# Performance work log

Hardware: AMD Instinct MI355X
Metric: run time of the kernel (lower is better)

## Reference

```python
import jax, jax.numpy as jnp
import numpy as np

B, L, D = 2, 2048, 1024
H, DH = 16, 64
SCALE = 1.0 / np.sqrt(DH).astype(np.float32)
NEG = -1e9


def setup_inputs() -> dict:
    key = jax.random.key(0)
    ks = jax.random.split(key, 12)
    s = 0.02
    x = jax.random.normal(ks[0], (B, L, D), jnp.float32)
    lattice = jax.random.normal(ks[1], (B, 6), jnp.float32)
    B_graph = jax.random.normal(ks[2], (B, L, L), jnp.float32) * 0.05
    # causal additive mask [L, L]
    attn_mask = jnp.where(jnp.tril(jnp.ones((L, L), bool)), 0.0, NEG).astype(jnp.float32)
    Wq = jax.random.normal(ks[3], (D, H * DH), jnp.float32) * s
    bq = jnp.zeros((H * DH,), jnp.float32)
    Wk = jax.random.normal(ks[4], (D, H * DH), jnp.float32) * s
    bk = jnp.zeros((H * DH,), jnp.float32)
    Wv = jax.random.normal(ks[5], (D, H * DH), jnp.float32) * s
    bv = jnp.zeros((H * DH,), jnp.float32)
    Wo = jax.random.normal(ks[6], (H * DH, D), jnp.float32) * s
    bo = jnp.zeros((D,), jnp.float32)
    Wl = jax.random.normal(ks[7], (6, H), jnp.float32) * s
    bl = jnp.zeros((H,), jnp.float32)
    return {"x": x, "lattice": lattice, "B_graph": B_graph, "attn_mask": attn_mask,
            "Wq": Wq, "bq": bq, "Wk": Wk, "bk": bk, "Wv": Wv, "bv": bv,
            "Wo": Wo, "bo": bo, "Wl": Wl, "bl": bl}


def reference(x, lattice, B_graph, attn_mask, Wq, bq, Wk, bk, Wv, bv, Wo, bo, Wl, bl):
    b, l, d = x.shape
    # projections -> [b, h, l, dh]
    q = (x @ Wq + bq).reshape(b, l, H, DH).transpose(0, 2, 1, 3)
    k = (x @ Wk + bk).reshape(b, l, H, DH).transpose(0, 2, 1, 3)
    v = (x @ Wv + bv).reshape(b, l, H, DH).transpose(0, 2, 1, 3)
    scores = jnp.einsum('bhid,bhjd->bhij', q, k) * SCALE
    lattice_bias = lattice @ Wl + bl          # [b, h]
    scores = scores + lattice_bias[:, :, None, None]
    scores = scores + B_graph[:, None, :, :]   # [b,1,l,l]
    scores = scores + attn_mask[None, None, :, :]
    attn = jax.nn.softmax(scores.astype(jnp.float32), axis=-1).astype(scores.dtype)
    out = jnp.einsum('bhij,bhjd->bhid', attn, v)
    out = out.transpose(0, 2, 1, 3).reshape(b, l, H * DH)
    out = out @ Wo + bo
    return (out, attn)
```

## Files before the change

kernel.cpp:

```cpp
#include <hip/hip_runtime.h>
#include <stdint.h>
#include <stddef.h>

#define BB 2
#define LL 2048
#define DD 1024
#define HH 16
#define DHH 64
#define NH 1024

typedef __attribute__((ext_vector_type(8))) __bf16 bf16x8;
typedef __attribute__((ext_vector_type(4))) float f32x4;

__device__ __forceinline__ f32x4 mfma_bf16(bf16x8 a, bf16x8 b, f32x4 c) {
    return __builtin_amdgcn_mfma_f32_16x16x32_bf16(a, b, c, 0, 0, 0);
}

__device__ __forceinline__ unsigned short f2bf(float f) {
    union { float f; unsigned u; } v; v.f = f;
    unsigned r = v.u + 0x7FFFu + ((v.u >> 16) & 1u);
    return (unsigned short)(r >> 16);
}

__device__ __forceinline__ float bf2f(unsigned short s) {
    union { unsigned u; float f; } v; v.u = ((unsigned)s) << 16;
    return v.f;
}

__device__ __forceinline__ bf16x8 ld_frag(const unsigned short* p) {
    return *reinterpret_cast<const bf16x8*>(p);
}

__global__ __launch_bounds__(256)
void conv_x_kernel(const float* __restrict__ x, unsigned short* __restrict__ xb)
{
    const size_t i = ((size_t)blockIdx.x * 256 + threadIdx.x) * 8;
    float4 a = *(const float4*)(x + i);
    float4 b = *(const float4*)(x + i + 4);
    unsigned short t[8];
    t[0] = f2bf(a.x); t[1] = f2bf(a.y); t[2] = f2bf(a.z); t[3] = f2bf(a.w);
    t[4] = f2bf(b.x); t[5] = f2bf(b.y); t[6] = f2bf(b.z); t[7] = f2bf(b.w);
    *(int4*)(xb + i) = *(const int4*)t;
}

__global__ __launch_bounds__(256)
void conv_w_kernel(const float* __restrict__ W0, const float* __restrict__ W1,
                   const float* __restrict__ W2, const float* __restrict__ W3,
                   unsigned short* __restrict__ Wqkvt,
                   unsigned short* __restrict__ Wot)
{
    __shared__ unsigned short Ls[64][72];
    const int which = blockIdx.z;
    const float* W = (which == 0) ? W0 : (which == 1) ? W1 : (which == 2) ? W2 : W3;
    unsigned short* Wt = (which == 3) ? Wot : (Wqkvt + (size_t)which * 1024 * 1024);

    const int kt = blockIdx.x * 64, nt = blockIdx.y * 64;
    const int tid = threadIdx.x;

    {
        const int r = tid >> 2, c = (tid & 3) * 16;
        const float* wp = W + (size_t)(kt + r) * 1024 + nt + c;
        unsigned short t[16];
#pragma unroll
        for (int q = 0; q < 4; ++q) {
            float4 f = *(const float4*)(wp + q * 4);
            t[q * 4 + 0] = f2bf(f.x); t[q * 4 + 1] = f2bf(f.y);
            t[q * 4 + 2] = f2bf(f.z); t[q * 4 + 3] = f2bf(f.w);
        }
        *(int4*)&Ls[r][c]     = *(const int4*)&t[0];
        *(int4*)&Ls[r][c + 8] = *(const int4*)&t[8];
    }
    __syncthreads();
    {
        const int nr = tid >> 2, kc = (tid & 3) * 16;
        unsigned short t[16];
#pragma unroll
        for (int m = 0; m < 16; ++m) t[m] = Ls[kc + m][nr];
        unsigned short* op = Wt + (size_t)(nt + nr) * 1024 + kt + kc;
        *(int4*)op       = *(const int4*)&t[0];
        *(int4*)(op + 8) = *(const int4*)&t[8];
    }
}

template<int MODE>
__global__ __launch_bounds__(256)
void gemm128_kernel(const unsigned short* __restrict__ A,
                    const unsigned short* __restrict__ Bt,
                    const float* __restrict__ b0, const float* __restrict__ b1,
                    const float* __restrict__ b2,
                    void* __restrict__ outp)
{
    __shared__ __align__(16) unsigned short As[128][64];
    __shared__ __align__(16) unsigned short Bs[128][64];

    const int tid  = threadIdx.x;
    const int lane = tid & 63;
    const int w    = tid >> 6;
    const int wr   = w >> 1, wc = w & 1;
    const int l16  = lane & 15, lk = lane >> 4;

    const int m0 = blockIdx.y * 128;
    const int n0 = blockIdx.x * 128;

    const int r8  = tid >> 3;
    const int cb  = tid & 7;
    const int swz = cb ^ (r8 & 7);

    const unsigned short* Ap = A  + (size_t)m0 * 1024 + cb * 8;
    const unsigned short* Bp = Bt + (size_t)n0 * 1024 + cb * 8;

    f32x4 acc[4][4];
#pragma unroll
    for (int i = 0; i < 4; ++i)
#pragma unroll
        for (int j = 0; j < 4; ++j) acc[i][j] = f32x4{0.f, 0.f, 0.f, 0.f};

    for (int k0 = 0; k0 < 1024; k0 += 64) {
        __syncthreads();
#pragma unroll
        for (int c = 0; c < 4; ++c) {
            const int row = c * 32 + r8;
            bf16x8 av = ld_frag(Ap + (size_t)row * 1024 + k0);
            bf16x8 bv = ld_frag(Bp + (size_t)row * 1024 + k0);
            *(bf16x8*)&As[row][swz * 8] = av;
            *(bf16x8*)&Bs[row][swz * 8] = bv;
        }
        __syncthreads();

#pragma unroll
        for (int kk = 0; kk < 2; ++kk) {
            bf16x8 af[4], bfr[4];
#pragma unroll
            for (int fm = 0; fm < 4; ++fm) {
                const int row = wr * 64 + fm * 16 + l16;
                const int kb  = kk * 4 + lk;
                af[fm] = ld_frag(&As[row][(kb ^ (row & 7)) * 8]);
            }
#pragma unroll
            for (int fn = 0; fn < 4; ++fn) {
                const int row = wc * 64 + fn * 16 + l16;
                const int kb  = kk * 4 + lk;
                bfr[fn] = ld_frag(&Bs[row][(kb ^ (row & 7)) * 8]);
            }
#pragma unroll
            for (int fm = 0; fm < 4; ++fm)
#pragma unroll
                for (int fn = 0; fn < 4; ++fn)
                    acc[fm][fn] = mfma_bf16(af[fm], bfr[fn], acc[fm][fn]);
        }
    }

    if (MODE == 0) {
        const int which = n0 >> 10;
        const float* bias = (which == 0) ? b0 : (which == 1) ? b1 : b2;
        unsigned short* out = (unsigned short*)outp
                            + (size_t)which * ((size_t)BB * HH * LL * DHH);
        const int c00 = n0 & 1023;
#pragma unroll
        for (int fm = 0; fm < 4; ++fm)
#pragma unroll
            for (int fn = 0; fn < 4; ++fn)
#pragma unroll
                for (int r = 0; r < 4; ++r) {
                    const int grow = m0 + wr * 64 + fm * 16 + lk * 4 + r;
                    const int c    = c00 + wc * 64 + fn * 16 + l16;
                    const float v  = acc[fm][fn][r] + bias[c];
                    const int b = grow >> 11, i = grow & 2047;
                    const int h = c >> 6,     d = c & 63;
                    out[(((size_t)(b * HH + h)) * LL + i) * DHH + d] = f2bf(v);
                }
    } else {
        float* out = (float*)outp;
#pragma unroll
        for (int fm = 0; fm < 4; ++fm)
#pragma unroll
            for (int fn = 0; fn < 4; ++fn)
#pragma unroll
                for (int r = 0; r < 4; ++r) {
                    const int grow = m0 + wr * 64 + fm * 16 + lk * 4 + r;
                    const int gcol = n0 + wc * 64 + fn * 16 + l16;
                    out[(size_t)grow * DD + gcol] = acc[fm][fn][r] + b0[gcol];
                }
    }
}

__global__ __launch_bounds__(256)
void v_transpose_kernel(const unsigned short* __restrict__ vws,
                        unsigned short* __restrict__ vT)
{
    __shared__ unsigned short Ls[64][72];
    const int bh = blockIdx.y;
    const int i0 = blockIdx.x * 64;
    const int tid = threadIdx.x;

    {
        const int r = tid >> 2, c = (tid & 3) * 16;
        const unsigned short* vp = vws + ((size_t)bh * LL + i0 + r) * DHH + c;
        *(int4*)&Ls[r][c]     = *(const int4*)vp;
        *(int4*)&Ls[r][c + 8] = *(const int4*)(vp + 8);
    }
    __syncthreads();
    {
        const int d = tid >> 2, c = (tid & 3) * 16;
        unsigned short tmp[16];
#pragma unroll
        for (int m = 0; m < 16; ++m) tmp[m] = Ls[c + m][d];
        unsigned short* op = vT + ((size_t)bh * DHH + d) * LL + i0 + c;
        *(int4*)op       = *(const int4*)&tmp[0];
        *(int4*)(op + 8) = *(const int4*)&tmp[8];
    }
}


#define LOADK(KB, JB) do {                                                     \
    const unsigned short* kt_ = kbase + (size_t)(JB) * 64 * DHH;               \
    _Pragma("unroll")                                                          \
    for (int fn = 0; fn < 4; ++fn) {                                           \
        KB[2 * fn]     = ld_frag(kt_ + (size_t)(fn * 16 + l16) * DHH + lk * 8);\
        KB[2 * fn + 1] = ld_frag(kt_ + (size_t)(fn * 16 + l16) * DHH + 32 + lk * 8);\
    }                                                                          \
} while (0)

#define ACCUMA(JB, KB) do {                                                    \
    float g_[16];                                                              \
    _Pragma("unroll")                                                          \
    for (int fn = 0; fn < 4; ++fn) {                                           \
        const float* gp_ = gbrow + (JB) * 64 + fn * 16 + l16;                  \
        _Pragma("unroll")                                                      \
        for (int r = 0; r < 4; ++r) g_[fn * 4 + r] = gp_[(size_t)r * LL];      \
    }                                                                          \
    f32x4 z_[4];                                                               \
    _Pragma("unroll")                                                          \
    for (int fn = 0; fn < 4; ++fn) {                                           \
        f32x4 z = {0.f, 0.f, 0.f, 0.f};                                        \
        z = mfma_bf16(qa0, KB[2 * fn], z);                                     \
        z = mfma_bf16(qa1, KB[2 * fn + 1], z);                                 \
        z_[fn] = z;                                                            \
    }                                                                          \
    _Pragma("unroll")                                                          \
    for (int fn = 0; fn < 4; ++fn) {                                           \
        const int gj_ = (JB) * 64 + fn * 16 + l16;                             \
        _Pragma("unroll")                                                      \
        for (int r = 0; r < 4; ++r) {                                          \
            const float sv_ = fmaf(z_[fn][r], 0.125f, lb + g_[fn * 4 + r]);    \
            s_run[r] += (gj_ > gi0 + r) ? 0.f : __expf(sv_);                   \
        }                                                                      \
    }                                                                          \
} while (0)

__global__ __launch_bounds__(128, 4)
void attn_kernel(const unsigned short* __restrict__ qws,
                 const unsigned short* __restrict__ kws,
                 const unsigned short* __restrict__ vT,
                 const float* __restrict__ B_graph,
                 const float* __restrict__ lattice,
                 const float* __restrict__ Wl,
                 const float* __restrict__ bl,
                 float* __restrict__ attn_out,
                 unsigned short* __restrict__ out_pre)
{
    const int n  = blockIdx.x;
    const int bh = n & 31;
    const int tb = n >> 5;
    const int kg = tb >> 3, tt = tb & 7;
    const int ib = 8 * kg + ((kg & 1) ? 7 - tt : tt);
    const int b = bh >> 4, h = bh & 15;
    const int i0 = ib * 32;
    const int nj = (ib >> 1) + 1;

    __shared__ unsigned short Ps[2][16][72];

    const int tid  = threadIdx.x;
    const int lane = tid & 63;
    const int w    = tid >> 6;
    const int l16  = lane & 15, lk = lane >> 4;

    float lb = bl[h];
#pragma unroll
    for (int t = 0; t < 6; ++t) lb += lattice[b * 6 + t] * Wl[t * HH + h];

    const int bhh = b * HH + h;
    const unsigned short* qbase = qws + ((size_t)bhh * LL + i0) * DHH;
    const unsigned short* kbase = kws + (size_t)bhh * LL * DHH;
    const unsigned short* vtb   = vT + (size_t)bhh * DHH * LL;
    const float* gb = B_graph + (size_t)b * LL * LL;

    bf16x8 qa0 = ld_frag(qbase + (size_t)(w * 16 + l16) * DHH + lk * 8);
    bf16x8 qa1 = ld_frag(qbase + (size_t)(w * 16 + l16) * DHH + 32 + lk * 8);

    const int gi0 = i0 + w * 16 + lk * 4;
    const float* gbrow = gb + (size_t)gi0 * LL;

    float s_run[4];
#pragma unroll
    for (int r = 0; r < 4; ++r) s_run[r] = 0.f;

    {
        bf16x8 ka[8], kb[8];
        LOADK(ka, 0);
        int jb = 1;
        for (; jb + 1 < nj; jb += 2) {
            LOADK(kb, jb);
            ACCUMA(jb - 1, ka);
            LOADK(ka, jb + 1);
            ACCUMA(jb, kb);
        }
        if (jb < nj) {
            LOADK(kb, jb);
            ACCUMA(jb - 1, ka);
            ACCUMA(jb, kb);
        } else {
            ACCUMA(jb - 1, ka);
        }
    }
#pragma unroll
    for (int off = 1; off < 16; off <<= 1)
#pragma unroll
        for (int r = 0; r < 4; ++r) s_run[r] += __shfl_xor(s_run[r], off, 64);

    float inv_s[4];
#pragma unroll
    for (int r = 0; r < 4; ++r) inv_s[r] = 1.0f / s_run[r];

    f32x4 oacc[4];
#pragma unroll
    for (int fn = 0; fn < 4; ++fn) oacc[fn] = f32x4{0.f, 0.f, 0.f, 0.f};

    for (int jb = 0; jb < nj; ++jb) {
        bf16x8 ka[8];
        LOADK(ka, jb);

        bf16x8 vb[8];
#pragma unroll
        for (int fn = 0; fn < 4; ++fn) {
            const unsigned short* vp_ = vtb + (size_t)(fn * 16 + l16) * LL + jb * 64;
            vb[2 * fn]     = ld_frag(vp_ + lk * 8);
            vb[2 * fn + 1] = ld_frag(vp_ + 32 + lk * 8);
        }
        float g_[16];
#pragma unroll
        for (int fn = 0; fn < 4; ++fn) {
            const float* gp_ = gbrow + jb * 64 + fn * 16 + l16;
#pragma unroll
            for (int r = 0; r < 4; ++r) g_[fn * 4 + r] = gp_[(size_t)r * LL];
        }

        f32x4 z_[4];
#pragma unroll
        for (int fn = 0; fn < 4; ++fn) {
            f32x4 z = {0.f, 0.f, 0.f, 0.f};
            z = mfma_bf16(qa0, ka[2 * fn], z);
            z = mfma_bf16(qa1, ka[2 * fn + 1], z);
            z_[fn] = z;
        }
#pragma unroll
        for (int fn = 0; fn < 4; ++fn) {
            const int gj = jb * 64 + fn * 16 + l16;
#pragma unroll
            for (int r = 0; r < 4; ++r) {
                const float sv = fmaf(z_[fn][r], 0.125f, lb + g_[fn * 4 + r]);
                const float p = ((gj > gi0 + r) ? 0.f : __expf(sv)) * inv_s[r];
                Ps[w][lk * 4 + r][fn * 16 + l16] = f2bf(p);
            }
        }

        const int jc0 = jb * 64 + l16 * 4;
#pragma unroll
        for (int s = 0; s < 4; ++s) {
            const int row = s * 4 + lk;
            const int gi  = i0 + w * 16 + row;
            ushort4 pb = *(const ushort4*)&Ps[w][row][l16 * 4];
            f32x4 pv;
            pv.x = bf2f(pb.x); pv.y = bf2f(pb.y);
            pv.z = bf2f(pb.z); pv.w = bf2f(pb.w);
            __builtin_nontemporal_store(
                pv, (f32x4*)&attn_out[((size_t)bhh * LL + gi) * LL + jc0]);
        }

        bf16x8 pa0 = ld_frag(&Ps[w][l16][lk * 8]);
        bf16x8 pa1 = ld_frag(&Ps[w][l16][32 + lk * 8]);
#pragma unroll
        for (int fn = 0; fn < 4; ++fn) {
            oacc[fn] = mfma_bf16(pa0, vb[2 * fn], oacc[fn]);
            oacc[fn] = mfma_bf16(pa1, vb[2 * fn + 1], oacc[fn]);
        }
    }

    const int zc0 = nj * 64;
    if (zc0 < LL) {
        const int nz4 = (LL - zc0) >> 2;
        const f32x4 z4 = {0.f, 0.f, 0.f, 0.f};
        for (int row = 0; row < 32; ++row) {
            f32x4* zp = (f32x4*)(attn_out + ((size_t)bhh * LL + i0 + row) * LL + zc0);
            for (int c4 = tid; c4 < nz4; c4 += 128)
                __builtin_nontemporal_store(z4, &zp[c4]);
        }
    }

#pragma unroll
    for (int fn = 0; fn < 4; ++fn)
#pragma unroll
        for (int r = 0; r < 4; ++r) {
            const int gi = gi0 + r;
            const int d  = fn * 16 + l16;
            out_pre[((size_t)(b * LL + gi)) * NH + h * DHH + d] = f2bf(oacc[fn][r]);
        }
}

extern "C" void kernel_launch(void* const* d_in, const int* in_sizes, int n_in,
                              void* d_out, int out_size, void* d_ws, size_t ws_size,
                              hipStream_t stream)
{
    const float* x       = (const float*)d_in[0];
    const float* lattice = (const float*)d_in[1];
    const float* B_graph = (const float*)d_in[2];
    const float* Wq = (const float*)d_in[4];
    const float* bq = (const float*)d_in[5];
    const float* Wk = (const float*)d_in[6];
    const float* bk = (const float*)d_in[7];
    const float* Wv = (const float*)d_in[8];
    const float* bv = (const float*)d_in[9];
    const float* Wo = (const float*)d_in[10];
    const float* bo = (const float*)d_in[11];
    const float* Wl = (const float*)d_in[12];
    const float* bl = (const float*)d_in[13];

    float* out  = (float*)d_out;
    float* attn = out + (size_t)BB * LL * DD;

    const size_t PHL = (size_t)BB * HH * LL * DHH;
    unsigned short* qkv    = (unsigned short*)d_ws;
    unsigned short* qw     = qkv;
    unsigned short* kw     = qkv + PHL;
    unsigned short* vw     = qkv + 2 * PHL;
    unsigned short* outpre = qkv + 3 * PHL;
    unsigned short* Wqkvt  = outpre;
    unsigned short* xb     = outpre + (size_t)BB * LL * NH;
    unsigned short* vT     = xb;
    unsigned short* Wot    = xb + (size_t)BB * LL * DD;

    conv_x_kernel<<<dim3((BB * LL * DD) / (256 * 8)), 256, 0, stream>>>(x, xb);
    conv_w_kernel<<<dim3(16, 16, 4), 256, 0, stream>>>(Wq, Wk, Wv, Wo, Wqkvt, Wot);

    gemm128_kernel<0><<<dim3(3 * NH / 128, (BB * LL) / 128), 256, 0, stream>>>(
        xb, Wqkvt, bq, bk, bv, qkv);

    v_transpose_kernel<<<dim3(LL / 64, BB * HH), 256, 0, stream>>>(vw, vT);

    attn_kernel<<<dim3(BB * HH * (LL / 32)), 128, 0, stream>>>(
        qw, kw, vT, B_graph, lattice, Wl, bl, attn, outpre);

    gemm128_kernel<1><<<dim3(DD / 128, (BB * LL) / 128), 256, 0, stream>>>(
        outpre, Wot, bo, bo, bo, out);
}
```

Baseline: 317.8 us.

## Transpose QK^T MFMA so each lane owns a query row with contiguous columns

Swaps the MFMA operand order for the score computation so each lane holds four consecutive key columns of a single query row. B_graph can then be read as float4 vectors and attn written straight from registers, with no bf16 round trip through LDS. The row-sum reduction drops from a four-step shuffle over four values to two shuffles of one value. A side effect is that the stored attn values are now full fp32 rather than bf16-rounded, while the P@V path still uses bf16 staged in LDS with a different write pattern.

```diff
diff --git a/kernel.cpp b/kernel.cpp
--- a/kernel.cpp
+++ b/kernel.cpp
@@ -20,11 +20,6 @@
     union { float f; unsigned u; } v; v.f = f;
     unsigned r = v.u + 0x7FFFu + ((v.u >> 16) & 1u);
     return (unsigned short)(r >> 16);
-}
-
-__device__ __forceinline__ float bf2f(unsigned short s) {
-    union { unsigned u; float f; } v; v.u = ((unsigned)s) << 16;
-    return v.f;
 }
 
 __device__ __forceinline__ bf16x8 ld_frag(const unsigned short* p) {
@@ -222,28 +217,25 @@
 } while (0)
 
 #define ACCUMA(JB, KB) do {                                                    \
-    float g_[16];                                                              \
+    f32x4 gv_[4];                                                              \
     _Pragma("unroll")                                                          \
-    for (int fn = 0; fn < 4; ++fn) {                                           \
-        const float* gp_ = gbrow + (JB) * 64 + fn * 16 + l16;                  \
-        _Pragma("unroll")                                                      \
-        for (int r = 0; r < 4; ++r) g_[fn * 4 + r] = gp_[(size_t)r * LL];      \
-    }                                                                          \
+    for (int fn = 0; fn < 4; ++fn)                                             \
+        gv_[fn] = *(const f32x4*)(gbrow + (JB) * 64 + fn * 16 + lk * 4);       \
     f32x4 z_[4];                                                               \
     _Pragma("unroll")                                                          \
     for (int fn = 0; fn < 4; ++fn) {                                           \
         f32x4 z = {0.f, 0.f, 0.f, 0.f};                                        \
-        z = mfma_bf16(qa0, KB[2 * fn], z);                                     \
-        z = mfma_bf16(qa1, KB[2 * fn + 1], z);                                 \
+        z = mfma_bf16(KB[2 * fn], qa0, z);                                     \
+        z = mfma_bf16(KB[2 * fn + 1], qa1, z);                                 \
         z_[fn] = z;                                                            \
     }                                                                          \
     _Pragma("unroll")                                                          \
     for (int fn = 0; fn < 4; ++fn) {                                           \
-        const int gj_ = (JB) * 64 + fn * 16 + l16;                             \
         _Pragma("unroll")                                                      \
         for (int r = 0; r < 4; ++r) {                                          \
-            const float sv_ = fmaf(z_[fn][r], 0.125f, lb + g_[fn * 4 + r]);    \
-            s_run[r] += (gj_ > gi0 + r) ? 0.f : __expf(sv_);                   \
+            const int gj_ = (JB) * 64 + fn * 16 + lk * 4 + r;                  \
+            const float sv_ = fmaf(z_[fn][r], 0.125f, lb + gv_[fn][r]);        \
+            s_run += (gj_ > gqi) ? 0.f : __expf(sv_);                          \
         }                                                                      \
     }                                                                          \
 } while (0)
@@ -288,12 +280,12 @@
     bf16x8 qa0 = ld_frag(qbase + (size_t)(w * 16 + l16) * DHH + lk * 8);
     bf16x8 qa1 = ld_frag(qbase + (size_t)(w * 16 + l16) * DHH + 32 + lk * 8);
 
-    const int gi0 = i0 + w * 16 + lk * 4;
-    const float* gbrow = gb + (size_t)gi0 * LL;
-
-    float s_run[4];
-#pragma unroll
-    for (int r = 0; r < 4; ++r) s_run[r] = 0.f;
+    const int gqi = i0 + w * 16 + l16;
+    const int goi = i0 + w * 16 + lk * 4;
+    const float* gbrow = gb + (size_t)gqi * LL;
+    float* arow = attn_out + ((size_t)bhh * LL + gqi) * LL;
+
+    float s_run = 0.f;
 
     {
         bf16x8 ka[8], kb[8];
@@ -313,14 +305,9 @@
             ACCUMA(jb - 1, ka);
         }
     }
-#pragma unroll
-    for (int off = 1; off < 16; off <<= 1)
-#pragma unroll
-        for (int r = 0; r < 4; ++r) s_run[r] += __shfl_xor(s_run[r], off, 64);
-
-    float inv_s[4];
-#pragma unroll
-    for (int r = 0; r < 4; ++r) inv_s[r] = 1.0f / s_run[r];
+    s_run += __shfl_xor(s_run, 16, 64);
+    s_run += __shfl_xor(s_run, 32, 64);
+    const float inv_s = 1.0f / s_run;
 
     f32x4 oacc[4];
 #pragma unroll
@@ -337,44 +324,35 @@
             vb[2 * fn]     = ld_frag(vp_ + lk * 8);
             vb[2 * fn + 1] = ld_frag(vp_ + 32 + lk * 8);
         }
-        float g_[16];
-#pragma unroll
-        for (int fn = 0; fn < 4; ++fn) {
-            const float* gp_ = gbrow + jb * 64 + fn * 16 + l16;
-#pragma unroll
-            for (int r = 0; r < 4; ++r) g_[fn * 4 + r] = gp_[(size_t)r * LL];
-        }
+        f32x4 gv_[4];
+#pragma unroll
+        for (int fn = 0; fn < 4; ++fn)
+            gv_[fn] = *(const f32x4*)(gbrow + jb * 64 + fn * 16 + lk * 4);
 
         f32x4 z_[4];
 #pragma unroll
         for (int fn = 0; fn < 4; ++fn) {
             f32x4 z = {0.f, 0.f, 0.f, 0.f};
-            z = mfma_bf16(qa0, ka[2 * fn], z);
-            z = mfma_bf16(qa1, ka[2 * fn + 1], z);
+            z = mfma_bf16(ka[2 * fn], qa0, z);
+            z = mfma_bf16(ka[2 * fn + 1], qa1, z);
             z_[fn] = z;
         }
+
 #pragma unroll
         for (int fn = 0; fn < 4; ++fn) {
-            const int gj = jb * 64 + fn * 16 + l16;
+            f32x4 pv;
 #pragma unroll
             for (int r = 0; r < 4; ++r) {
-                const float sv = fmaf(z_[fn][r], 0.125f, lb + g_[fn * 4 + r]);
-                const float p = ((gj > gi0 + r) ? 0.f : __expf(sv)) * inv_s[r];
-                Ps[w][lk * 4 + r][fn * 16 + l16] = f2bf(p);
+                const int gj = jb * 64 + fn * 16 + lk * 4 + r;
+                const float sv = fmaf(z_[fn][r], 0.125f, lb + gv_[fn][r]);
+                pv[r] = ((gj > gqi) ? 0.f : __expf(sv)) * inv_s;
             }
-        }
-
-        const int jc0 = jb * 64 + l16 * 4;
-#pragma unroll
-        for (int s = 0; s < 4; ++s) {
-            const int row = s * 4 + lk;
-            const int gi  = i0 + w * 16 + row;
-            ushort4 pb = *(const ushort4*)&Ps[w][row][l16 * 4];
-            f32x4 pv;
-            pv.x = bf2f(pb.x); pv.y = bf2f(pb.y);
-            pv.z = bf2f(pb.z); pv.w = bf2f(pb.w);
             __builtin_nontemporal_store(
-                pv, (f32x4*)&attn_out[((size_t)bhh * LL + gi) * LL + jc0]);
+                pv, (f32x4*)(arow + jb * 64 + fn * 16 + lk * 4));
+            ushort4 pb;
+            pb.x = f2bf(pv.x); pb.y = f2bf(pv.y);
+            pb.z = f2bf(pv.z); pb.w = f2bf(pv.w);
+            *(ushort4*)&Ps[w][l16][fn * 16 + lk * 4] = pb;
         }
 
         bf16x8 pa0 = ld_frag(&Ps[w][l16][lk * 8]);
@@ -401,7 +379,7 @@
     for (int fn = 0; fn < 4; ++fn)
 #pragma unroll
         for (int r = 0; r < 4; ++r) {
-            const int gi = gi0 + r;
+            const int gi = goi + r;
             const int d  = fn * 16 + l16;
             out_pre[((size_t)(b * LL + gi)) * NH + h * DHH + d] = f2bf(oacc[fn][r]);
         }
```

Measured after the change: 344.9 us. +8.5%, slower.
